# Kernel optimization log

Hardware: AMD Instinct MI355X
Metric: run time of the kernel (lower is better)

Reference implementation:

```python
import jax, jax.numpy as jnp
import numpy as np

D_IN = 1024
D_OUT = 1024
NUM_HEADS = 16
HEAD_DIM = D_OUT // NUM_HEADS


def setup_inputs() -> dict:
    key = jax.random.key(0)
    ks = jax.random.split(key, 6)
    s = 0.02
    return {
        "x": jax.random.normal(ks[0], (4, 2048, D_IN), dtype=jnp.float32),
        "Wq": jax.random.normal(ks[1], (D_IN, D_OUT), dtype=jnp.float32) * s,
        "Wk": jax.random.normal(ks[2], (D_IN, D_OUT), dtype=jnp.float32) * s,
        "Wv": jax.random.normal(ks[3], (D_IN, D_OUT), dtype=jnp.float32) * s,
        "Wo": jax.random.normal(ks[4], (D_OUT, D_OUT), dtype=jnp.float32) * s,
        "bo": jax.random.normal(ks[5], (D_OUT,), dtype=jnp.float32) * s,
    }


def reference(x, Wq, Wk, Wv, Wo, bo):
    B, S, _ = x.shape
    # QKV projections (no bias), split into heads: [B, H, S, Dh]
    def split_heads(t):
        return t.reshape(B, S, NUM_HEADS, HEAD_DIM).transpose(0, 2, 1, 3)

    q = split_heads(x @ Wq)
    k = split_heads(x @ Wk)
    v = split_heads(x @ Wv)

    # causal scores [B, H, S, S]; note: original masks BEFORE scaling,
    # but -inf is scale-invariant so softmax(scores/sqrt(d)) with mask is identical.
    scores = jnp.einsum("bhqd,bhkd->bhqk", q, k) / jnp.sqrt(jnp.asarray(HEAD_DIM, x.dtype))
    causal = jnp.tril(jnp.ones((S, S), dtype=bool))
    scores = jnp.where(causal, scores, -jnp.inf)
    attn = jax.nn.softmax(scores, axis=-1)
    # dropout p=0.0 -> identity
    ctx = jnp.einsum("bhqk,bhkd->bhqd", attn, v)  # [B, H, S, Dh]
    ctx = ctx.transpose(0, 2, 1, 3).reshape(B, S, D_OUT)
    return ctx @ Wo + bo
```

## Files before the change

### kernel.cpp

```cpp
#include <hip/hip_runtime.h>
#include <hip/hip_bf16.h>
#include <math.h>


typedef __attribute__((ext_vector_type(8))) short short8;
typedef __attribute__((ext_vector_type(4))) float f32x4;

#define MFMA_BF16(a, b, c) __builtin_amdgcn_mfma_f32_16x16x32_bf16((a), (b), (c), 0, 0, 0)

__device__ __forceinline__ void gld_lds16(const void* g, void* l) {
  __builtin_amdgcn_global_load_lds((const __attribute__((address_space(1))) void*)g,
                                   (__attribute__((address_space(3))) void*)l, 16, 0, 0);
}

__global__ void prep_kernel(const float* __restrict__ x, __hip_bfloat16* __restrict__ xb,
                            const float* __restrict__ W0, const float* __restrict__ W1,
                            const float* __restrict__ W2, const float* __restrict__ W3,
                            __hip_bfloat16* __restrict__ T0, __hip_bfloat16* __restrict__ T1,
                            __hip_bfloat16* __restrict__ T2, __hip_bfloat16* __restrict__ T3) {
  const int bid = blockIdx.x, tid = threadIdx.x;
  if (bid < 8192) {
    int i = bid * 256 + tid;
    float4 v = ((const float4*)x)[i];
    __align__(8) __hip_bfloat16 tmp[4] = {__float2bfloat16(v.x), __float2bfloat16(v.y),
                                          __float2bfloat16(v.z), __float2bfloat16(v.w)};
    ((ushort4*)xb)[i] = *(const ushort4*)tmp;
  } else {
    int zz = bid - 8192;
    int z = zz >> 10, rem = zz & 1023;
    const float* W = (z == 0) ? W0 : (z == 1) ? W1 : (z == 2) ? W2 : W3;
    __hip_bfloat16* Wt = (z == 0) ? T0 : (z == 1) ? T1 : (z == 2) ? T2 : T3;
    __shared__ float tile[32][33];
    int tx = tid & 31, ty = tid >> 5;
    int n0 = (rem & 31) * 32, k0 = (rem >> 5) * 32;
#pragma unroll
    for (int i = 0; i < 4; ++i)
      tile[ty + i * 8][tx] = W[(size_t)(k0 + ty + i * 8) * 1024 + n0 + tx];
    __syncthreads();
#pragma unroll
    for (int i = 0; i < 4; ++i)
      Wt[(size_t)(n0 + ty + i * 8) * 1024 + k0 + tx] = __float2bfloat16(tile[tx][ty + i * 8]);
  }
}

__global__ __launch_bounds__(256, 2) void gemm_qkv(
    const __hip_bfloat16* __restrict__ A, const __hip_bfloat16* __restrict__ Bt,
    __hip_bfloat16* __restrict__ q, __hip_bfloat16* __restrict__ k,
    __hip_bfloat16* __restrict__ vT) {
  __shared__ __align__(16) __hip_bfloat16 As[128 * 64];
  __shared__ __align__(16) __hip_bfloat16 Bs[128 * 64];
  const int tid = threadIdx.x;
  const int lane = tid & 63, wid = tid >> 6;
  const int quad = lane >> 4, l16 = lane & 15;
  const int part = blockIdx.x >> 3;
  const int n0 = (blockIdx.x & 7) * 128;
  const int gn0 = part * 1024 + n0;
  const int m0 = blockIdx.y * 128;
  const int wm = (wid & 1) * 64, wn = (wid >> 1) * 64;
  const int swz = l16 & 7;

  f32x4 acc[4][4] = {};

  for (int k0 = 0; k0 < 1024; k0 += 64) {
    __syncthreads();
#pragma unroll
    for (int i = 0; i < 4; ++i) {
      int sbase = __builtin_amdgcn_readfirstlane(wid * 256 + i * 64);
      int s = sbase + lane;
      int row = s >> 3;
      int ch = (s & 7) ^ (row & 7);
      gld_lds16(A + (size_t)(m0 + row) * 1024 + k0 + ch * 8, &As[sbase * 8]);
      gld_lds16(Bt + (size_t)(gn0 + row) * 1024 + k0 + ch * 8, &Bs[sbase * 8]);
    }
    __syncthreads();

    short8 af[4][2], bfr[4][2];
#pragma unroll
    for (int t = 0; t < 4; ++t)
#pragma unroll
      for (int kc = 0; kc < 2; ++kc) {
        int chp = (kc * 4 + quad) ^ swz;
        af[t][kc]  = *(const short8*)&As[(wm + t * 16 + l16) * 64 + chp * 8];
        bfr[t][kc] = *(const short8*)&Bs[(wn + t * 16 + l16) * 64 + chp * 8];
      }
#pragma unroll
    for (int kc = 0; kc < 2; ++kc)
#pragma unroll
      for (int mt = 0; mt < 4; ++mt)
#pragma unroll
        for (int nt = 0; nt < 4; ++nt)
          acc[mt][nt] = MFMA_BF16(af[mt][kc], bfr[nt][kc], acc[mt][nt]);
  }

  const float CSCL = 0.18033688011112042f;
  if (part < 2) {
    __hip_bfloat16* C = (part == 0) ? q : k;
    const float scl = (part == 0) ? CSCL : 1.0f;
#pragma unroll
    for (int mt = 0; mt < 4; ++mt)
#pragma unroll
      for (int nt = 0; nt < 4; ++nt) {
        int row = m0 + wm + mt * 16 + quad * 4;
        int col = n0 + wn + nt * 16 + l16;
#pragma unroll
        for (int r = 0; r < 4; ++r)
          C[(size_t)(row + r) * 1024 + col] = __float2bfloat16(acc[mt][nt][r] * scl);
      }
  } else {
#pragma unroll
    for (int mt = 0; mt < 4; ++mt)
#pragma unroll
      for (int nt = 0; nt < 4; ++nt) {
        int row = m0 + wm + mt * 16 + quad * 4;
        int nn = n0 + wn + nt * 16 + l16;
        __align__(8) __hip_bfloat16 p4[4];
#pragma unroll
        for (int r = 0; r < 4; ++r) p4[r] = __float2bfloat16(acc[mt][nt][r]);
        *(ushort4*)(vT + (size_t)nn * 8192 + row) = *(const ushort4*)p4;
      }
  }
}

__global__ __launch_bounds__(256, 2) void gemm_bt_f32out(
    const __hip_bfloat16* __restrict__ A, const __hip_bfloat16* __restrict__ Bt,
    float* __restrict__ C, const float* __restrict__ bias, int M, int N, int K) {
  __shared__ __align__(16) __hip_bfloat16 As[128 * 64];
  __shared__ __align__(16) __hip_bfloat16 Bs[128 * 64];
  const int tid = threadIdx.x;
  const int lane = tid & 63, wid = tid >> 6;
  const int quad = lane >> 4, l16 = lane & 15;
  const int m0 = blockIdx.y * 128, n0 = blockIdx.x * 128;
  const int wm = (wid & 1) * 64, wn = (wid >> 1) * 64;
  const int swz = l16 & 7;

  f32x4 acc[4][4] = {};

  for (int k0 = 0; k0 < K; k0 += 64) {
    __syncthreads();
#pragma unroll
    for (int i = 0; i < 4; ++i) {
      int sbase = __builtin_amdgcn_readfirstlane(wid * 256 + i * 64);
      int s = sbase + lane;
      int row = s >> 3;
      int ch = (s & 7) ^ (row & 7);
      gld_lds16(A + (size_t)(m0 + row) * K + k0 + ch * 8, &As[sbase * 8]);
      gld_lds16(Bt + (size_t)(n0 + row) * K + k0 + ch * 8, &Bs[sbase * 8]);
    }
    __syncthreads();

    short8 af[4][2], bfr[4][2];
#pragma unroll
    for (int t = 0; t < 4; ++t)
#pragma unroll
      for (int kc = 0; kc < 2; ++kc) {
        int chp = (kc * 4 + quad) ^ swz;
        af[t][kc]  = *(const short8*)&As[(wm + t * 16 + l16) * 64 + chp * 8];
        bfr[t][kc] = *(const short8*)&Bs[(wn + t * 16 + l16) * 64 + chp * 8];
      }
#pragma unroll
    for (int kc = 0; kc < 2; ++kc)
#pragma unroll
      for (int mt = 0; mt < 4; ++mt)
#pragma unroll
        for (int nt = 0; nt < 4; ++nt)
          acc[mt][nt] = MFMA_BF16(af[mt][kc], bfr[nt][kc], acc[mt][nt]);
  }

#pragma unroll
  for (int mt = 0; mt < 4; ++mt)
#pragma unroll
    for (int nt = 0; nt < 4; ++nt) {
      int row = m0 + wm + mt * 16 + quad * 4;
      int col = n0 + wn + nt * 16 + l16;
      float b = bias[col];
#pragma unroll
      for (int r = 0; r < 4; ++r)
        C[(size_t)(row + r) * N + col] = acc[mt][nt][r] + b;
    }
}

__global__ __launch_bounds__(256, 2) void attn_kernel(
    const __hip_bfloat16* __restrict__ Q, const __hip_bfloat16* __restrict__ Km,
    const __hip_bfloat16* __restrict__ vT, __hip_bfloat16* __restrict__ ctx) {
  const int bid = blockIdx.x;
  const int p = bid & 7, h = (bid >> 3) & 15, b = bid >> 7;
  const size_t rbase = (size_t)b * 2048;
  const int tid = threadIdx.x, lane = tid & 63, wid = tid >> 6;
  const int quad = lane >> 4, l16 = lane & 15;

  __shared__ __align__(16) __hip_bfloat16 Ks[64 * 72];
  __shared__ __align__(16) __hip_bfloat16 Vs[64 * 72];
  __shared__ __align__(16) __hip_bfloat16 Ps[4][32 * 76];

  const float NEG_BIG = -1e30f;

#pragma unroll 1
  for (int sub = 0; sub < 2; ++sub) {
    const int qt = sub ? (15 - p) : p;
    const int q0 = qt * 128;

    short8 qf[2][2];
#pragma unroll
    for (int mt = 0; mt < 2; ++mt)
#pragma unroll
      for (int kc = 0; kc < 2; ++kc)
        qf[mt][kc] = *(const short8*)(Q + (rbase + q0 + wid * 32 + mt * 16 + l16) * 1024 +
                                      h * 64 + kc * 32 + quad * 8);

    f32x4 o[2][4] = {};
    f32x4 lp[2] = {};
    const int wave_max_row = q0 + wid * 32 + 31;
    const int ktiles = q0 / 64 + 2;

#pragma unroll 1
    for (int kt = 0; kt < ktiles; ++kt) {
      const int kbase = kt * 64;
      __syncthreads();
      {
#pragma unroll
        for (int i = 0; i < 2; ++i) {
          int s = tid + i * 256;
          int krow = s >> 3, ch = s & 7;
          *(short8*)&Ks[krow * 72 + ch * 8] =
              *(const short8*)(Km + (rbase + kbase + krow) * 1024 + h * 64 + ch * 8);
        }
      }
      {
#pragma unroll
        for (int i = 0; i < 2; ++i) {
          int s = tid + i * 256;
          int d = s >> 3, ch = s & 7;
          *(short8*)&Vs[d * 72 + ch * 8] =
              *(const short8*)(vT + (size_t)(h * 64 + d) * 8192 + rbase + kbase + ch * 8);
        }
      }
      __syncthreads();

      if (kbase <= wave_max_row) {
        short8 kf[4][2];
#pragma unroll
        for (int nt = 0; nt < 4; ++nt)
#pragma unroll
          for (int kc = 0; kc < 2; ++kc)
            kf[nt][kc] = *(const short8*)&Ks[(nt * 16 + l16) * 72 + kc * 32 + quad * 8];
        f32x4 s[2][4];
#pragma unroll
        for (int mt = 0; mt < 2; ++mt)
#pragma unroll
          for (int nt = 0; nt < 4; ++nt) {
            f32x4 sv = {0.f, 0.f, 0.f, 0.f};
            sv = MFMA_BF16(qf[mt][0], kf[nt][0], sv);
            sv = MFMA_BF16(qf[mt][1], kf[nt][1], sv);
            s[mt][nt] = sv;
          }
        if (kbase + 63 > q0 + wid * 32) {
#pragma unroll
          for (int mt = 0; mt < 2; ++mt)
#pragma unroll
            for (int nt = 0; nt < 4; ++nt)
#pragma unroll
              for (int r = 0; r < 4; ++r) {
                int row = q0 + wid * 32 + mt * 16 + quad * 4 + r;
                int col = kbase + nt * 16 + l16;
                if (col > row) s[mt][nt][r] = NEG_BIG;
              }
        }
#pragma unroll
        for (int mt = 0; mt < 2; ++mt) {
#pragma unroll
          for (int nt = 0; nt < 4; ++nt)
#pragma unroll
            for (int r = 0; r < 4; ++r) {
              float pv = __builtin_amdgcn_exp2f(s[mt][nt][r]);
              s[mt][nt][r] = pv;
              lp[mt][r] += pv;
            }
#pragma unroll
          for (int nt = 0; nt < 4; ++nt)
#pragma unroll
            for (int r = 0; r < 4; ++r)
              Ps[wid][(mt * 16 + quad * 4 + r) * 76 + nt * 16 + l16] =
                  __float2bfloat16(s[mt][nt][r]);
        }
        short8 pa[2][2], vf[4][2];
#pragma unroll
        for (int mt = 0; mt < 2; ++mt)
#pragma unroll
          for (int ch = 0; ch < 2; ++ch)
            pa[mt][ch] = *(const short8*)&Ps[wid][(mt * 16 + l16) * 76 + ch * 32 + quad * 8];
#pragma unroll
        for (int dt = 0; dt < 4; ++dt)
#pragma unroll
          for (int ch = 0; ch < 2; ++ch)
            vf[dt][ch] = *(const short8*)&Vs[(dt * 16 + l16) * 72 + ch * 32 + quad * 8];
#pragma unroll
        for (int mt = 0; mt < 2; ++mt)
#pragma unroll
          for (int dt = 0; dt < 4; ++dt) {
            o[mt][dt] = MFMA_BF16(pa[mt][0], vf[dt][0], o[mt][dt]);
            o[mt][dt] = MFMA_BF16(pa[mt][1], vf[dt][1], o[mt][dt]);
          }
      }
    }

#pragma unroll
    for (int mt = 0; mt < 2; ++mt) {
#pragma unroll
      for (int msk = 1; msk <= 8; msk <<= 1)
#pragma unroll
        for (int r = 0; r < 4; ++r)
          lp[mt][r] += __shfl_xor(lp[mt][r], msk, 64);
      float inv[4];
#pragma unroll
      for (int r = 0; r < 4; ++r) inv[r] = 1.f / lp[mt][r];
#pragma unroll
      for (int dt = 0; dt < 4; ++dt)
#pragma unroll
        for (int r = 0; r < 4; ++r)
          ctx[(rbase + q0 + wid * 32 + mt * 16 + quad * 4 + r) * 1024 + h * 64 + dt * 16 + l16] =
              __float2bfloat16(o[mt][dt][r] * inv[r]);
    }
  }
}

extern "C" void kernel_launch(void* const* d_in, const int* in_sizes, int n_in,
                              void* d_out, int out_size, void* d_ws, size_t ws_size,
                              hipStream_t stream) {
  const float* x  = (const float*)d_in[0];
  const float* Wq = (const float*)d_in[1];
  const float* Wk = (const float*)d_in[2];
  const float* Wv = (const float*)d_in[3];
  const float* Wo = (const float*)d_in[4];
  const float* bo = (const float*)d_in[5];
  float* out = (float*)d_out;

  char* ws = (char*)d_ws;
  const size_t MB = 1024ull * 1024ull;
  __hip_bfloat16* q   = (__hip_bfloat16*)(ws);
  __hip_bfloat16* k   = (__hip_bfloat16*)(ws + 16 * MB);
  __hip_bfloat16* vT  = (__hip_bfloat16*)(ws + 32 * MB);
  __hip_bfloat16* woT = (__hip_bfloat16*)(ws + 48 * MB);
  __hip_bfloat16* ctx = q;

  char* outc = (char*)d_out;
  __hip_bfloat16* xb    = (__hip_bfloat16*)(outc);
  __hip_bfloat16* wcatT = (__hip_bfloat16*)(outc + 16 * MB);

  prep_kernel<<<8192 + 4096, 256, 0, stream>>>(
      x, xb, Wq, Wk, Wv, Wo,
      wcatT, wcatT + 1024 * 1024, wcatT + 2048 * 1024, woT);

  gemm_qkv<<<dim3(24, 64), 256, 0, stream>>>(xb, wcatT, q, k, vT);

  attn_kernel<<<512, 256, 0, stream>>>(q, k, vT, ctx);

  gemm_bt_f32out<<<dim3(8, 64), 256, 0, stream>>>(ctx, woT, out, bo, 8192, 1024, 1024);
}
```

Baseline: 248.0 us.

## Shrink attention query tile, swizzle LDS, use direct-to-LDS loads and XCD-aware mapping

The attention kernel changes from 128-row to 64-row query tiles (16 rows per wave) and doubles the grid to 1024 blocks, pairing tiles t and 31-t to balance causal work. K and V tiles are now loaded with global_load_lds into unpadded LDS buffers using an XOR swizzle, and the P buffer uses the same swizzle. Block IDs are remapped so all query tiles for one (batch, head) land on the same XCD to improve L2 reuse of K/V. Launch bounds are raised to 4 blocks per CU for higher occupancy. In exchange, K/V tile loads per query row double, since each tile now serves half as many query rows.

```diff
diff --git a/kernel.cpp b/kernel.cpp
--- a/kernel.cpp
+++ b/kernel.cpp
@@ -179,147 +179,107 @@
     }
 }
 
-__global__ __launch_bounds__(256, 2) void attn_kernel(
+__global__ __launch_bounds__(256, 4) void attn_kernel(
     const __hip_bfloat16* __restrict__ Q, const __hip_bfloat16* __restrict__ Km,
     const __hip_bfloat16* __restrict__ vT, __hip_bfloat16* __restrict__ ctx) {
   const int bid = blockIdx.x;
-  const int p = bid & 7, h = (bid >> 3) & 15, b = bid >> 7;
+  const int xcd = bid & 7, loc = bid >> 3;
+  const int grp = xcd * 8 + (loc >> 4);
+  const int p = loc & 15;
+  const int h = grp & 15, b = grp >> 4;
   const size_t rbase = (size_t)b * 2048;
   const int tid = threadIdx.x, lane = tid & 63, wid = tid >> 6;
   const int quad = lane >> 4, l16 = lane & 15;
-
-  __shared__ __align__(16) __hip_bfloat16 Ks[64 * 72];
-  __shared__ __align__(16) __hip_bfloat16 Vs[64 * 72];
-  __shared__ __align__(16) __hip_bfloat16 Ps[4][32 * 76];
+  const int sw = l16 & 7;
+
+  __shared__ __align__(16) __hip_bfloat16 Ks[64 * 64];
+  __shared__ __align__(16) __hip_bfloat16 Vs[64 * 64];
+  __shared__ __align__(16) __hip_bfloat16 Ps[4][16 * 64];
 
   const float NEG_BIG = -1e30f;
 
 #pragma unroll 1
   for (int sub = 0; sub < 2; ++sub) {
-    const int qt = sub ? (15 - p) : p;
-    const int q0 = qt * 128;
-
-    short8 qf[2][2];
-#pragma unroll
-    for (int mt = 0; mt < 2; ++mt)
-#pragma unroll
-      for (int kc = 0; kc < 2; ++kc)
-        qf[mt][kc] = *(const short8*)(Q + (rbase + q0 + wid * 32 + mt * 16 + l16) * 1024 +
-                                      h * 64 + kc * 32 + quad * 8);
-
-    f32x4 o[2][4] = {};
-    f32x4 lp[2] = {};
-    const int wave_max_row = q0 + wid * 32 + 31;
-    const int ktiles = q0 / 64 + 2;
+    const int t = sub ? (31 - p) : p;
+    const int q0 = t * 64;
+
+    short8 qf[2];
+#pragma unroll
+    for (int kc = 0; kc < 2; ++kc)
+      qf[kc] = *(const short8*)(Q + (rbase + q0 + wid * 16 + l16) * 1024 +
+                                h * 64 + kc * 32 + quad * 8);
+
+    f32x4 o[4] = {};
+    f32x4 lp = {};
 
 #pragma unroll 1
-    for (int kt = 0; kt < ktiles; ++kt) {
+    for (int kt = 0; kt <= t; ++kt) {
       const int kbase = kt * 64;
       __syncthreads();
-      {
-#pragma unroll
-        for (int i = 0; i < 2; ++i) {
-          int s = tid + i * 256;
-          int krow = s >> 3, ch = s & 7;
-          *(short8*)&Ks[krow * 72 + ch * 8] =
-              *(const short8*)(Km + (rbase + kbase + krow) * 1024 + h * 64 + ch * 8);
+#pragma unroll
+      for (int i = 0; i < 2; ++i) {
+        int sbase = __builtin_amdgcn_readfirstlane(i * 256 + wid * 64);
+        int s = sbase + lane;
+        int row = s >> 3;
+        int lch = (s & 7) ^ (row & 7);
+        gld_lds16(Km + (rbase + kbase + row) * 1024 + h * 64 + lch * 8, &Ks[sbase * 8]);
+        gld_lds16(vT + (size_t)(h * 64 + row) * 8192 + rbase + kbase + lch * 8,
+                  &Vs[sbase * 8]);
+      }
+      __syncthreads();
+
+      f32x4 sv[4];
+#pragma unroll
+      for (int nt = 0; nt < 4; ++nt) {
+        short8 k0 = *(const short8*)&Ks[(nt * 16 + l16) * 64 + ((quad ^ sw) << 3)];
+        short8 k1 = *(const short8*)&Ks[(nt * 16 + l16) * 64 + (((4 + quad) ^ sw) << 3)];
+        f32x4 z = {0.f, 0.f, 0.f, 0.f};
+        z = MFMA_BF16(qf[0], k0, z);
+        z = MFMA_BF16(qf[1], k1, z);
+        sv[nt] = z;
+      }
+      if (kt == t) {
+#pragma unroll
+        for (int nt = 0; nt < 4; ++nt)
+#pragma unroll
+          for (int r = 0; r < 4; ++r)
+            if (nt * 16 + l16 > wid * 16 + quad * 4 + r) sv[nt][r] = NEG_BIG;
+      }
+#pragma unroll
+      for (int nt = 0; nt < 4; ++nt)
+#pragma unroll
+        for (int r = 0; r < 4; ++r) {
+          float pv = __builtin_amdgcn_exp2f(sv[nt][r]);
+          lp[r] += pv;
+          int rrow = quad * 4 + r;
+          int cph = (nt * 2 + (l16 >> 3)) ^ (rrow & 7);
+          Ps[wid][rrow * 64 + cph * 8 + (l16 & 7)] = __float2bfloat16(pv);
         }
-      }
-      {
-#pragma unroll
-        for (int i = 0; i < 2; ++i) {
-          int s = tid + i * 256;
-          int d = s >> 3, ch = s & 7;
-          *(short8*)&Vs[d * 72 + ch * 8] =
-              *(const short8*)(vT + (size_t)(h * 64 + d) * 8192 + rbase + kbase + ch * 8);
-        }
-      }
-      __syncthreads();
-
-      if (kbase <= wave_max_row) {
-        short8 kf[4][2];
-#pragma unroll
-        for (int nt = 0; nt < 4; ++nt)
-#pragma unroll
-          for (int kc = 0; kc < 2; ++kc)
-            kf[nt][kc] = *(const short8*)&Ks[(nt * 16 + l16) * 72 + kc * 32 + quad * 8];
-        f32x4 s[2][4];
-#pragma unroll
-        for (int mt = 0; mt < 2; ++mt)
-#pragma unroll
-          for (int nt = 0; nt < 4; ++nt) {
-            f32x4 sv = {0.f, 0.f, 0.f, 0.f};
-            sv = MFMA_BF16(qf[mt][0], kf[nt][0], sv);
-            sv = MFMA_BF16(qf[mt][1], kf[nt][1], sv);
-            s[mt][nt] = sv;
-          }
-        if (kbase + 63 > q0 + wid * 32) {
-#pragma unroll
-          for (int mt = 0; mt < 2; ++mt)
-#pragma unroll
-            for (int nt = 0; nt < 4; ++nt)
-#pragma unroll
-              for (int r = 0; r < 4; ++r) {
-                int row = q0 + wid * 32 + mt * 16 + quad * 4 + r;
-                int col = kbase + nt * 16 + l16;
-                if (col > row) s[mt][nt][r] = NEG_BIG;
-              }
-        }
-#pragma unroll
-        for (int mt = 0; mt < 2; ++mt) {
-#pragma unroll
-          for (int nt = 0; nt < 4; ++nt)
-#pragma unroll
-            for (int r = 0; r < 4; ++r) {
-              float pv = __builtin_amdgcn_exp2f(s[mt][nt][r]);
-              s[mt][nt][r] = pv;
-              lp[mt][r] += pv;
-            }
-#pragma unroll
-          for (int nt = 0; nt < 4; ++nt)
-#pragma unroll
-            for (int r = 0; r < 4; ++r)
-              Ps[wid][(mt * 16 + quad * 4 + r) * 76 + nt * 16 + l16] =
-                  __float2bfloat16(s[mt][nt][r]);
-        }
-        short8 pa[2][2], vf[4][2];
-#pragma unroll
-        for (int mt = 0; mt < 2; ++mt)
-#pragma unroll
-          for (int ch = 0; ch < 2; ++ch)
-            pa[mt][ch] = *(const short8*)&Ps[wid][(mt * 16 + l16) * 76 + ch * 32 + quad * 8];
-#pragma unroll
-        for (int dt = 0; dt < 4; ++dt)
-#pragma unroll
-          for (int ch = 0; ch < 2; ++ch)
-            vf[dt][ch] = *(const short8*)&Vs[(dt * 16 + l16) * 72 + ch * 32 + quad * 8];
-#pragma unroll
-        for (int mt = 0; mt < 2; ++mt)
-#pragma unroll
-          for (int dt = 0; dt < 4; ++dt) {
-            o[mt][dt] = MFMA_BF16(pa[mt][0], vf[dt][0], o[mt][dt]);
-            o[mt][dt] = MFMA_BF16(pa[mt][1], vf[dt][1], o[mt][dt]);
-          }
+      short8 pa0 = *(const short8*)&Ps[wid][l16 * 64 + ((quad ^ sw) << 3)];
+      short8 pa1 = *(const short8*)&Ps[wid][l16 * 64 + (((4 + quad) ^ sw) << 3)];
+#pragma unroll
+      for (int dt = 0; dt < 4; ++dt) {
+        short8 v0 = *(const short8*)&Vs[(dt * 16 + l16) * 64 + ((quad ^ sw) << 3)];
+        short8 v1 = *(const short8*)&Vs[(dt * 16 + l16) * 64 + (((4 + quad) ^ sw) << 3)];
+        o[dt] = MFMA_BF16(pa0, v0, o[dt]);
+        o[dt] = MFMA_BF16(pa1, v1, o[dt]);
       }
     }
 
 #pragma unroll
-    for (int mt = 0; mt < 2; ++mt) {
-#pragma unroll
-      for (int msk = 1; msk <= 8; msk <<= 1)
-#pragma unroll
-        for (int r = 0; r < 4; ++r)
-          lp[mt][r] += __shfl_xor(lp[mt][r], msk, 64);
-      float inv[4];
-#pragma unroll
-      for (int r = 0; r < 4; ++r) inv[r] = 1.f / lp[mt][r];
-#pragma unroll
-      for (int dt = 0; dt < 4; ++dt)
-#pragma unroll
-        for (int r = 0; r < 4; ++r)
-          ctx[(rbase + q0 + wid * 32 + mt * 16 + quad * 4 + r) * 1024 + h * 64 + dt * 16 + l16] =
-              __float2bfloat16(o[mt][dt][r] * inv[r]);
-    }
+    for (int msk = 1; msk <= 8; msk <<= 1)
+#pragma unroll
+      for (int r = 0; r < 4; ++r)
+        lp[r] += __shfl_xor(lp[r], msk, 64);
+    float inv[4];
+#pragma unroll
+    for (int r = 0; r < 4; ++r) inv[r] = 1.f / lp[r];
+#pragma unroll
+    for (int dt = 0; dt < 4; ++dt)
+#pragma unroll
+      for (int r = 0; r < 4; ++r)
+        ctx[(rbase + q0 + wid * 16 + quad * 4 + r) * 1024 + h * 64 + dt * 16 + l16] =
+            __float2bfloat16(o[dt][r] * inv[r]);
   }
 }
 
@@ -352,7 +312,7 @@
 
   gemm_qkv<<<dim3(24, 64), 256, 0, stream>>>(xb, wcatT, q, k, vT);
 
-  attn_kernel<<<512, 256, 0, stream>>>(q, k, vT, ctx);
+  attn_kernel<<<1024, 256, 0, stream>>>(q, k, vT, ctx);
 
   gemm_bt_f32out<<<dim3(8, 64), 256, 0, stream>>>(ctx, woT, out, bo, 8192, 1024, 1024);
 }
```

Result: slower. 253.9 us (+2.4%).

## Double-buffer K/V tiles with async LDS loads, XOR swizzle, and XCD-aware block mapping

Applied to the files above, without the earlier changes.

The attention kernel now prefetches the next K/V tile into a second LDS buffer with global_load_lds while the current tile is being computed, which removes one barrier per iteration. Padded LDS rows are replaced by an XOR-swizzled 64-wide layout to avoid bank conflicts. The S=QK^T MFMA operands are swapped so each lane holds one query row, which lets P be written as packed 4-element stores and cuts the row-sum shuffles. Block indices are remapped so blocks of the same (batch, head) land on the same XCD for L2 reuse. The cost is double the K/V LDS footprint and more subtle synchronization.

```diff
diff --git a/kernel.cpp b/kernel.cpp
--- a/kernel.cpp
+++ b/kernel.cpp
@@ -183,116 +183,130 @@
     const __hip_bfloat16* __restrict__ Q, const __hip_bfloat16* __restrict__ Km,
     const __hip_bfloat16* __restrict__ vT, __hip_bfloat16* __restrict__ ctx) {
   const int bid = blockIdx.x;
-  const int p = bid & 7, h = (bid >> 3) & 15, b = bid >> 7;
+  const int xcd = bid & 7, loc = bid >> 3;
+  const int grp = xcd * 8 + (loc >> 3);
+  const int p = loc & 7;
+  const int h = grp & 15, b = grp >> 4;
   const size_t rbase = (size_t)b * 2048;
   const int tid = threadIdx.x, lane = tid & 63, wid = tid >> 6;
   const int quad = lane >> 4, l16 = lane & 15;
-
-  __shared__ __align__(16) __hip_bfloat16 Ks[64 * 72];
-  __shared__ __align__(16) __hip_bfloat16 Vs[64 * 72];
-  __shared__ __align__(16) __hip_bfloat16 Ps[4][32 * 76];
+  const int sw = l16 & 7;
+
+  __shared__ __align__(16) __hip_bfloat16 Ks[2][64 * 64];
+  __shared__ __align__(16) __hip_bfloat16 Vs[2][64 * 64];
+  __shared__ __align__(16) __hip_bfloat16 Ps[4][32 * 64];
 
   const float NEG_BIG = -1e30f;
 
 #pragma unroll 1
   for (int sub = 0; sub < 2; ++sub) {
-    const int qt = sub ? (15 - p) : p;
-    const int q0 = qt * 128;
+    const int t = sub ? (15 - p) : p;
+    const int q0 = t * 128;
+    const int qw = q0 + wid * 32;
+    const int nkt = 2 * t + 2;
+
+    __syncthreads();
+    {
+#pragma unroll
+      for (int i = 0; i < 2; ++i) {
+        int sbase = __builtin_amdgcn_readfirstlane(i * 256 + wid * 64);
+        int s = sbase + lane, row = s >> 3, lch = (s & 7) ^ (row & 7);
+        gld_lds16(Km + (rbase + row) * 1024 + h * 64 + lch * 8, &Ks[0][sbase * 8]);
+        gld_lds16(vT + (size_t)(h * 64 + row) * 8192 + rbase + lch * 8, &Vs[0][sbase * 8]);
+      }
+    }
 
     short8 qf[2][2];
 #pragma unroll
     for (int mt = 0; mt < 2; ++mt)
 #pragma unroll
       for (int kc = 0; kc < 2; ++kc)
-        qf[mt][kc] = *(const short8*)(Q + (rbase + q0 + wid * 32 + mt * 16 + l16) * 1024 +
+        qf[mt][kc] = *(const short8*)(Q + (rbase + qw + mt * 16 + l16) * 1024 +
                                       h * 64 + kc * 32 + quad * 8);
 
     f32x4 o[2][4] = {};
-    f32x4 lp[2] = {};
-    const int wave_max_row = q0 + wid * 32 + 31;
-    const int ktiles = q0 / 64 + 2;
+    float lp[2] = {0.f, 0.f};
 
 #pragma unroll 1
-    for (int kt = 0; kt < ktiles; ++kt) {
+    for (int kt = 0; kt < nkt; ++kt) {
+      const int cur = kt & 1;
       const int kbase = kt * 64;
       __syncthreads();
-      {
+      if (kt + 1 < nkt) {
+        const int kb = kbase + 64;
 #pragma unroll
         for (int i = 0; i < 2; ++i) {
-          int s = tid + i * 256;
-          int krow = s >> 3, ch = s & 7;
-          *(short8*)&Ks[krow * 72 + ch * 8] =
-              *(const short8*)(Km + (rbase + kbase + krow) * 1024 + h * 64 + ch * 8);
+          int sbase = __builtin_amdgcn_readfirstlane(i * 256 + wid * 64);
+          int s = sbase + lane, row = s >> 3, lch = (s & 7) ^ (row & 7);
+          gld_lds16(Km + (rbase + kb + row) * 1024 + h * 64 + lch * 8,
+                    &Ks[cur ^ 1][sbase * 8]);
+          gld_lds16(vT + (size_t)(h * 64 + row) * 8192 + rbase + kb + lch * 8,
+                    &Vs[cur ^ 1][sbase * 8]);
         }
       }
-      {
-#pragma unroll
-        for (int i = 0; i < 2; ++i) {
-          int s = tid + i * 256;
-          int d = s >> 3, ch = s & 7;
-          *(short8*)&Vs[d * 72 + ch * 8] =
-              *(const short8*)(vT + (size_t)(h * 64 + d) * 8192 + rbase + kbase + ch * 8);
-        }
-      }
-      __syncthreads();
-
-      if (kbase <= wave_max_row) {
+      const __hip_bfloat16* Kb = &Ks[cur][0];
+      const __hip_bfloat16* Vb = &Vs[cur][0];
+
+      if (kbase <= qw + 31) {
         short8 kf[4][2];
 #pragma unroll
         for (int nt = 0; nt < 4; ++nt)
 #pragma unroll
           for (int kc = 0; kc < 2; ++kc)
-            kf[nt][kc] = *(const short8*)&Ks[(nt * 16 + l16) * 72 + kc * 32 + quad * 8];
-        f32x4 s[2][4];
+            kf[nt][kc] = *(const short8*)&Kb[(nt * 16 + l16) * 64 +
+                                             (((kc * 4 + quad) ^ sw) << 3)];
+        f32x4 sv[2][4];
 #pragma unroll
         for (int mt = 0; mt < 2; ++mt)
 #pragma unroll
           for (int nt = 0; nt < 4; ++nt) {
-            f32x4 sv = {0.f, 0.f, 0.f, 0.f};
-            sv = MFMA_BF16(qf[mt][0], kf[nt][0], sv);
-            sv = MFMA_BF16(qf[mt][1], kf[nt][1], sv);
-            s[mt][nt] = sv;
+            f32x4 z = {0.f, 0.f, 0.f, 0.f};
+            z = MFMA_BF16(kf[nt][0], qf[mt][0], z);
+            z = MFMA_BF16(kf[nt][1], qf[mt][1], z);
+            sv[mt][nt] = z;
           }
-        if (kbase + 63 > q0 + wid * 32) {
+        if (kbase + 63 > qw) {
 #pragma unroll
           for (int mt = 0; mt < 2; ++mt)
 #pragma unroll
             for (int nt = 0; nt < 4; ++nt)
 #pragma unroll
               for (int r = 0; r < 4; ++r) {
-                int row = q0 + wid * 32 + mt * 16 + quad * 4 + r;
-                int col = kbase + nt * 16 + l16;
-                if (col > row) s[mt][nt][r] = NEG_BIG;
+                int kpos = kbase + nt * 16 + quad * 4 + r;
+                int qrow = qw + mt * 16 + l16;
+                if (kpos > qrow) sv[mt][nt][r] = NEG_BIG;
               }
         }
 #pragma unroll
-        for (int mt = 0; mt < 2; ++mt) {
-#pragma unroll
-          for (int nt = 0; nt < 4; ++nt)
+        for (int mt = 0; mt < 2; ++mt)
+#pragma unroll
+          for (int nt = 0; nt < 4; ++nt) {
+            __align__(8) __hip_bfloat16 p4[4];
 #pragma unroll
             for (int r = 0; r < 4; ++r) {
-              float pv = __builtin_amdgcn_exp2f(s[mt][nt][r]);
-              s[mt][nt][r] = pv;
-              lp[mt][r] += pv;
+              float pv = __builtin_amdgcn_exp2f(sv[mt][nt][r]);
+              lp[mt] += pv;
+              p4[r] = __float2bfloat16(pv);
             }
-#pragma unroll
-          for (int nt = 0; nt < 4; ++nt)
-#pragma unroll
-            for (int r = 0; r < 4; ++r)
-              Ps[wid][(mt * 16 + quad * 4 + r) * 76 + nt * 16 + l16] =
-                  __float2bfloat16(s[mt][nt][r]);
-        }
-        short8 pa[2][2], vf[4][2];
+            int row = mt * 16 + l16;
+            int c16 = (nt * 2 + (quad >> 1)) ^ (row & 7);
+            *(ushort4*)&Ps[wid][row * 64 + c16 * 8 + (quad & 1) * 4] =
+                *(const ushort4*)p4;
+          }
+        short8 pa[2][2];
 #pragma unroll
         for (int mt = 0; mt < 2; ++mt)
 #pragma unroll
-          for (int ch = 0; ch < 2; ++ch)
-            pa[mt][ch] = *(const short8*)&Ps[wid][(mt * 16 + l16) * 76 + ch * 32 + quad * 8];
+          for (int kc = 0; kc < 2; ++kc)
+            pa[mt][kc] = *(const short8*)&Ps[wid][(mt * 16 + l16) * 64 +
+                                                  (((kc * 4 + quad) ^ sw) << 3)];
+        short8 vf[4][2];
 #pragma unroll
         for (int dt = 0; dt < 4; ++dt)
 #pragma unroll
-          for (int ch = 0; ch < 2; ++ch)
-            vf[dt][ch] = *(const short8*)&Vs[(dt * 16 + l16) * 72 + ch * 32 + quad * 8];
+          for (int kc = 0; kc < 2; ++kc)
+            vf[dt][kc] = *(const short8*)&Vb[(dt * 16 + l16) * 64 +
+                                             (((kc * 4 + quad) ^ sw) << 3)];
 #pragma unroll
         for (int mt = 0; mt < 2; ++mt)
 #pragma unroll
@@ -305,19 +319,20 @@
 
 #pragma unroll
     for (int mt = 0; mt < 2; ++mt) {
-#pragma unroll
-      for (int msk = 1; msk <= 8; msk <<= 1)
+      lp[mt] += __shfl_xor(lp[mt], 16, 64);
+      lp[mt] += __shfl_xor(lp[mt], 32, 64);
+    }
+#pragma unroll
+    for (int mt = 0; mt < 2; ++mt) {
+      float inv[4];
+#pragma unroll
+      for (int r = 0; r < 4; ++r)
+        inv[r] = 1.f / __shfl(lp[mt], quad * 4 + r, 64);
+#pragma unroll
+      for (int dt = 0; dt < 4; ++dt)
 #pragma unroll
         for (int r = 0; r < 4; ++r)
-          lp[mt][r] += __shfl_xor(lp[mt][r], msk, 64);
-      float inv[4];
-#pragma unroll
-      for (int r = 0; r < 4; ++r) inv[r] = 1.f / lp[mt][r];
-#pragma unroll
-      for (int dt = 0; dt < 4; ++dt)
-#pragma unroll
-        for (int r = 0; r < 4; ++r)
-          ctx[(rbase + q0 + wid * 32 + mt * 16 + quad * 4 + r) * 1024 + h * 64 + dt * 16 + l16] =
+          ctx[(rbase + qw + mt * 16 + quad * 4 + r) * 1024 + h * 64 + dt * 16 + l16] =
               __float2bfloat16(o[mt][dt][r] * inv[r]);
     }
   }
```

Result: faster. 237.7 us (-4.2%).
